# Kernel optimization log

Measured on AMD Instinct MI355X. Metric: run time of the kernel, lower is better.

Reference implementation:

```python
import math
import jax, jax.numpy as jnp
import numpy as np

B, D, H = 8, 2048, 256

def setup_inputs() -> dict:
    key = jax.random.key(0)
    ks = jax.random.split(key, 8)
    s = 1.0 / math.sqrt(H)
    x = jax.random.normal(ks[0], (B, D, H), dtype=jnp.float32)
    adj = jax.random.randint(ks[1], (B, D, D), 0, 2, dtype=jnp.int32)
    Wq = jax.random.normal(ks[2], (H, H), dtype=jnp.float32) * s
    Wk = jax.random.normal(ks[3], (H, H), dtype=jnp.float32) * s
    Wv = jax.random.normal(ks[4], (H, H), dtype=jnp.float32) * s
    Wp = jax.random.normal(ks[5], (H, H), dtype=jnp.float32) * s
    bp = jax.random.normal(ks[6], (H,), dtype=jnp.float32) * 0.01
    gamma = jnp.ones((H,), dtype=jnp.float32)
    beta = jnp.zeros((H,), dtype=jnp.float32)
    return {"x": x, "adj": adj, "Wq": Wq, "Wk": Wk, "Wv": Wv,
            "Wp": Wp, "bp": bp, "gamma": gamma, "beta": beta}

def _layer_norm(h, gamma, beta, eps=1e-5):
    mu = jnp.mean(h, axis=-1, keepdims=True)
    var = jnp.mean(jnp.square(h - mu), axis=-1, keepdims=True)
    return (h - mu) * jax.lax.rsqrt(var + eps) * gamma + beta

def reference(x, adj, Wq, Wk, Wv, Wp, bp, gamma, beta):
    # torch Linear: y = x @ W.T
    q = jnp.einsum('bdh,oh->bdo', x, Wq)
    k = jnp.einsum('bdh,oh->bdo', x, Wk)
    v = jnp.einsum('bdh,oh->bdo', x, Wv)
    scores = jnp.einsum('bdo,beo->bde', q, k) / math.sqrt(H)
    scores = jnp.where(adj <= 0, jnp.float32(-1e9), scores)
    attn = jax.nn.softmax(scores, axis=-1)
    agg = jnp.einsum('bde,beo->bdo', attn, v)
    out = jnp.einsum('bdo,po->bdp', agg, Wp) + bp
    return _layer_norm(x + out, gamma, beta)
```

## Files before the change

### kernel.cpp

```cpp
#include <hip/hip_runtime.h>
#include <stdint.h>

#define NB 8
#define ND 2048
#define NH 256

typedef __attribute__((ext_vector_type(8))) short bf16x8;
typedef __attribute__((ext_vector_type(4))) float f32x4;
typedef __attribute__((ext_vector_type(16))) float f32x16;
typedef __attribute__((ext_vector_type(4))) int   i32x4;
typedef __attribute__((ext_vector_type(2))) unsigned int u32x2;
typedef __attribute__((ext_vector_type(4))) unsigned int u32x4;

#define MFMA16 __builtin_amdgcn_mfma_f32_16x16x32_bf16
#define MFMA32 __builtin_amdgcn_mfma_f32_32x32x16_bf16

__device__ __forceinline__ unsigned short f2bf(float f) {
    union { float f; unsigned int u; } c; c.f = f;
    unsigned int u = c.u + 0x7FFFu + ((c.u >> 16) & 1u);
    return (unsigned short)(u >> 16);
}
__device__ __forceinline__ unsigned int pack2(float a, float b) {
    return (unsigned int)f2bf(a) | ((unsigned int)f2bf(b) << 16);
}
__device__ __forceinline__ unsigned int cvtpk(float a, float b) {
    unsigned int r;
    asm("v_cvt_pk_bf16_f32 %0, %1, %2" : "=v"(r) : "v"(a), "v"(b));
    return r;
}
__device__ __forceinline__ void plswap(unsigned int& a, unsigned int& b) {
    asm volatile("v_permlane32_swap_b32 %0, %1" : "+v"(a), "+v"(b));
}
__device__ __forceinline__ bf16x8 mk8(unsigned int a, unsigned int b, unsigned int c, unsigned int d) {
    union { unsigned int u[4]; bf16x8 v; } x;
    x.u[0] = a; x.u[1] = b; x.u[2] = c; x.u[3] = d;
    return x.v;
}
__device__ __forceinline__ void gload_lds16(const void* g, void* l) {
    __builtin_amdgcn_global_load_lds(
        (const __attribute__((address_space(1))) void*)g,
        (__attribute__((address_space(3))) void*)l, 16, 0, 0);
}
__device__ __forceinline__ float bflo(unsigned int u) { return __uint_as_float(u << 16); }
__device__ __forceinline__ float bfhi(unsigned int u) { return __uint_as_float(u & 0xffff0000u); }

__global__ __launch_bounds__(256) void qkv_kernel(
    const float* __restrict__ x,
    const float* __restrict__ Wq, const float* __restrict__ Wk, const float* __restrict__ Wv,
    unsigned short* __restrict__ qb, unsigned short* __restrict__ kb, unsigned short* __restrict__ vT)
{
    __shared__ unsigned short Wt[64][264];
    __shared__ unsigned short Xt[64][264];
    const int m0 = blockIdx.x * 64;
    const int o0 = blockIdx.y * 64;
    const int t = threadIdx.x;
    const int w = t >> 6, lane = t & 63, lr = lane & 15, half = lane >> 4;
    const int ar0 = 32 * (w >> 1), br0 = 32 * (w & 1);

#pragma unroll
    for (int i = 0; i < 16; ++i) {
        int fidx = i * 256 + t, row = fidx >> 6, c4 = fidx & 63;
        f32x4 vW = *reinterpret_cast<const f32x4*>(Wq + (size_t)(o0 + row) * NH + c4 * 4);
        f32x4 vX = *reinterpret_cast<const f32x4*>(x + (size_t)(m0 + row) * NH + c4 * 4);
        u32x2 pw; pw[0] = pack2(vW[0], vW[1]); pw[1] = pack2(vW[2], vW[3]);
        u32x2 px; px[0] = pack2(vX[0], vX[1]); px[1] = pack2(vX[2], vX[3]);
        *reinterpret_cast<u32x2*>(&Wt[row][c4 * 4]) = pw;
        *reinterpret_cast<u32x2*>(&Xt[row][c4 * 4]) = px;
    }
    __syncthreads();

    for (int z = 0; z < 3; ++z) {
        const unsigned short (*Ab)[264] = (z == 2) ? Xt : Wt;
        const unsigned short (*Bb)[264] = (z == 2) ? Wt : Xt;

        f32x4 acc[2][2] = {};
#pragma unroll
        for (int kk = 0; kk < 8; ++kk) {
            bf16x8 a[2], bfr[2];
#pragma unroll
            for (int f = 0; f < 2; ++f) {
                a[f]   = *reinterpret_cast<const bf16x8*>(&Ab[ar0 + 16 * f + lr][32 * kk + 8 * half]);
                bfr[f] = *reinterpret_cast<const bf16x8*>(&Bb[br0 + 16 * f + lr][32 * kk + 8 * half]);
            }
#pragma unroll
            for (int fa = 0; fa < 2; ++fa)
#pragma unroll
                for (int fb = 0; fb < 2; ++fb)
                    acc[fa][fb] = MFMA16(a[fa], bfr[fb], acc[fa][fb], 0, 0, 0);
        }

        if (z == 0) {
#pragma unroll
            for (int fa = 0; fa < 2; ++fa)
#pragma unroll
                for (int fb = 0; fb < 2; ++fb) {
                    int m = m0 + br0 + 16 * fb + lr;
                    int o = o0 + ar0 + 16 * fa + 4 * half;
                    u32x2 pk; pk[0] = pack2(acc[fa][fb][0], acc[fa][fb][1]);
                    pk[1] = pack2(acc[fa][fb][2], acc[fa][fb][3]);
                    *reinterpret_cast<u32x2*>(qb + (size_t)m * NH + o) = pk;
                }
        } else if (z == 1) {
#pragma unroll
            for (int fa = 0; fa < 2; ++fa)
#pragma unroll
                for (int fb = 0; fb < 2; ++fb) {
                    int m = m0 + br0 + 16 * fb + lr;
                    int o = o0 + ar0 + 16 * fa + 4 * half;
                    int bb = m >> 11, el = m & 2047;
                    u32x2 pk; pk[0] = pack2(acc[fa][fb][0], acc[fa][fb][1]);
                    pk[1] = pack2(acc[fa][fb][2], acc[fa][fb][3]);
                    size_t idx = (((size_t)bb * 32 + (o >> 3)) * 2048 + el) * 8 + (o & 7);
                    *reinterpret_cast<u32x2*>(kb + idx) = pk;
                }
        } else {
#pragma unroll
            for (int fa = 0; fa < 2; ++fa)
#pragma unroll
                for (int fb = 0; fb < 2; ++fb) {
                    int dg = m0 + ar0 + 16 * fa + 4 * half;
                    int o  = o0 + br0 + 16 * fb + lr;
                    int bb = dg >> 11, el = dg & 2047;
                    u32x2 pk; pk[0] = pack2(acc[fa][fb][0], acc[fa][fb][1]);
                    pk[1] = pack2(acc[fa][fb][2], acc[fa][fb][3]);
                    size_t idx = (((size_t)bb * 256 + (el >> 3)) * 256 + o) * 8 + (el & 7);
                    *reinterpret_cast<u32x2*>(vT + idx) = pk;
                }
        }

        if (z < 2) {
            __syncthreads();
            const float* Wn = (z == 0) ? Wk : Wv;
#pragma unroll
            for (int i = 0; i < 16; ++i) {
                int fidx = i * 256 + t, row = fidx >> 6, c4 = fidx & 63;
                f32x4 vW = *reinterpret_cast<const f32x4*>(Wn + (size_t)(o0 + row) * NH + c4 * 4);
                u32x2 pw; pw[0] = pack2(vW[0], vW[1]); pw[1] = pack2(vW[2], vW[3]);
                *reinterpret_cast<u32x2*>(&Wt[row][c4 * 4]) = pw;
            }
            __syncthreads();
        }
    }
}

template<int ESP, int SIDES>
__global__ __launch_bounds__(256, 2) void attn_kernel(
    const unsigned short* __restrict__ qb, const unsigned short* __restrict__ kb,
    const unsigned short* __restrict__ vT, const int* __restrict__ adj,
    unsigned short* __restrict__ part, float* __restrict__ mpart, float* __restrict__ lpart)
{
    constexpr int WAVES = 4;
    constexpr int GROUPS = WAVES / SIDES;
    constexpr int QB = 32 * GROUPS;
    constexpr int NOT = 8 / SIDES;
    constexpr int NT = (ND / ESP) / 32;

    __shared__ unsigned char KT[2][16384];
    __shared__ unsigned char VTl[2][16384];

    const int bid = blockIdx.x;
    const int b = bid & 7, es0 = (bid >> 3) & (ESP - 1), qt = bid / (8 * ESP);
    const int t = threadIdx.x, w = t >> 6, l = t & 63;
    const int lo32 = l & 31, hi = l >> 5;
    const int g = w & (GROUPS - 1), side = w / GROUPS;
    const int qbase = qt * QB + g * 32;
    const int obase = side * (256 / SIDES);
    const int ebase = es0 * (ND / ESP);
    const float SC = 0.0625f, L2E = 1.44269504f;

    bf16x8 qf[16];
    {
        const unsigned short* qr = qb + ((size_t)b * ND + qbase + lo32) * NH + 8 * hi;
#pragma unroll
        for (int kk = 0; kk < 16; ++kk)
            qf[kk] = *reinterpret_cast<const bf16x8*>(qr + kk * 16);
    }

    const char* kbc = (const char*)kb + ((size_t)b << 20);
    const char* vtc = (const char*)vT + ((size_t)b << 20);
    const int* adjr = adj + ((size_t)b * ND + qbase + lo32) * ND + ebase;

    auto stageK = [&](int buf, int tt) {
        const int e0s = ebase + tt * 32;
#pragma unroll
        for (int i = 0; i < 4; ++i) {
            int off = i * 4096 + t * 16;
            int koct = off >> 9, e = (off >> 4) & 31;
            gload_lds16(kbc + (size_t)koct * 32768 + (size_t)(e0s + e) * 16, &KT[buf][off]);
        }
    };
    auto stageV = [&](int buf, int tt) {
        const int Eb = (ebase + tt * 32) >> 3;
#pragma unroll
        for (int i = 0; i < 4; ++i) {
            int off = i * 4096 + t * 16;
            int eoct = off >> 12, o = (off >> 4) & 255;
            gload_lds16(vtc + (size_t)(Eb + eoct) * 4096 + (size_t)o * 16, &VTl[buf][off]);
        }
    };

    f32x16 acc[NOT] = {};
    float m_run = -__builtin_inff(), l_run = 0.f;

    stageK(0, 0); stageV(0, 0);
    __syncthreads();

    for (int tt = 0; tt < NT; ++tt) {
        const int cur = tt & 1;
        if (tt < NT - 1) { stageK(cur ^ 1, tt + 1); stageV(cur ^ 1, tt + 1); }

        i32x4 aj[4];
#pragma unroll
        for (int gg = 0; gg < 4; ++gg)
            aj[gg] = *reinterpret_cast<const i32x4*>(adjr + tt * 32 + gg * 8 + 4 * hi);

        const char* Kc = (const char*)&KT[cur][0];
        f32x16 sc = {};
#pragma unroll
        for (int kk = 0; kk < 16; ++kk) {
            bf16x8 kf = *reinterpret_cast<const bf16x8*>(Kc + kk * 1024 + hi * 512 + lo32 * 16);
            sc = MFMA32(kf, qf[kk], sc, 0, 0, 0);
        }

        float p[16];
        float tmax = -__builtin_inff();
#pragma unroll
        for (int gg = 0; gg < 4; ++gg)
#pragma unroll
            for (int r = 0; r < 4; ++r) {
                float sv = sc[gg * 4 + r] * SC;
                sv = (aj[gg][r] > 0) ? sv : -1e9f;
                p[gg * 4 + r] = sv;
                tmax = fmaxf(tmax, sv);
            }
        tmax = fmaxf(tmax, __shfl_xor(tmax, 32));
        if (!__all(tmax <= m_run + 8.0f)) {
            const float m_new = fmaxf(m_run, tmax);
            const float scale = exp2f((m_run - m_new) * L2E);
#pragma unroll
            for (int ot = 0; ot < NOT; ++ot)
#pragma unroll
                for (int r = 0; r < 16; ++r) acc[ot][r] *= scale;
            l_run *= scale;
            m_run = m_new;
        }
        float psum = 0.f;
#pragma unroll
        for (int r2 = 0; r2 < 16; ++r2) {
            float pe = exp2f((p[r2] - m_run) * L2E);
            p[r2] = pe;
            psum += pe;
        }
        psum += __shfl_xor(psum, 32);
        l_run += psum;

        unsigned int c0 = cvtpk(p[0], p[1]),   c1 = cvtpk(p[2], p[3]);
        unsigned int c2 = cvtpk(p[4], p[5]),   c3 = cvtpk(p[6], p[7]);
        plswap(c0, c2); plswap(c1, c3);
        unsigned int c4 = cvtpk(p[8], p[9]),   c5 = cvtpk(p[10], p[11]);
        unsigned int c6 = cvtpk(p[12], p[13]), c7 = cvtpk(p[14], p[15]);
        plswap(c4, c6); plswap(c5, c7);
        const bf16x8 pf0 = mk8(c0, c1, c2, c3);
        const bf16x8 pf1 = mk8(c4, c5, c6, c7);

        const char* Vc = (const char*)&VTl[cur][0];
#pragma unroll
        for (int ot = 0; ot < NOT; ++ot) {
            bf16x8 vf = *reinterpret_cast<const bf16x8*>(
                Vc + hi * 4096 + (size_t)(obase + ot * 32 + lo32) * 16);
            acc[ot] = MFMA32(vf, pf0, acc[ot], 0, 0, 0);
        }
#pragma unroll
        for (int ot = 0; ot < NOT; ++ot) {
            bf16x8 vf = *reinterpret_cast<const bf16x8*>(
                Vc + 8192 + hi * 4096 + (size_t)(obase + ot * 32 + lo32) * 16);
            acc[ot] = MFMA32(vf, pf1, acc[ot], 0, 0, 0);
        }
        __syncthreads();
    }

    const int qg = b * ND + qbase + lo32;
    unsigned short* pb = part + ((size_t)es0 * 16384 + qg) * 256;
#pragma unroll
    for (int ot = 0; ot < NOT; ++ot)
#pragma unroll
        for (int g2 = 0; g2 < 4; ++g2) {
            u32x2 pk;
            pk[0] = pack2(acc[ot][g2 * 4 + 0], acc[ot][g2 * 4 + 1]);
            pk[1] = pack2(acc[ot][g2 * 4 + 2], acc[ot][g2 * 4 + 3]);
            *reinterpret_cast<u32x2*>(pb + obase + ot * 32 + g2 * 8 + 4 * hi) = pk;
        }
    if (hi == 0 && side == 0) {
        mpart[(size_t)es0 * 16384 + qg] = m_run;
        lpart[(size_t)es0 * 16384 + qg] = l_run;
    }
}

template<int ESP>
__global__ __launch_bounds__(256) void fuse_kernel(
    const unsigned short* __restrict__ part, const float* __restrict__ mpart,
    const float* __restrict__ lpart, const float* __restrict__ Wp,
    const float* __restrict__ bp, const float* __restrict__ x,
    const float* __restrict__ gamma, const float* __restrict__ beta,
    float* __restrict__ out)
{
    __shared__ unsigned short Xt[64][264];
    __shared__ unsigned short Wt[64][264];
    __shared__ float hL[64][264];
    __shared__ float cel[64][ESP];

    const int M0 = blockIdx.x * 64;
    const int t = threadIdx.x;
    const float L2E = 1.44269504f;

    if (t < 64) {
        float me[ESP], le[ESP], M = -__builtin_inff();
#pragma unroll
        for (int e = 0; e < ESP; ++e) {
            me[e] = mpart[(size_t)e * 16384 + M0 + t];
            le[e] = lpart[(size_t)e * 16384 + M0 + t];
            M = fmaxf(M, me[e]);
        }
        float wsum = 0.f;
#pragma unroll
        for (int e = 0; e < ESP; ++e) { me[e] = exp2f((me[e] - M) * L2E); wsum += me[e] * le[e]; }
        const float inv = 1.f / wsum;
#pragma unroll
        for (int e = 0; e < ESP; ++e) cel[t][e] = me[e] * inv;
    }
#pragma unroll
    for (int i = 0; i < 16; ++i) {
        int fidx = i * 256 + t, row = fidx >> 6, c4 = fidx & 63;
        f32x4 vW = *reinterpret_cast<const f32x4*>(Wp + (size_t)row * NH + c4 * 4);
        u32x2 pw; pw[0] = pack2(vW[0], vW[1]); pw[1] = pack2(vW[2], vW[3]);
        *reinterpret_cast<u32x2*>(&Wt[row][c4 * 4]) = pw;
    }
    __syncthreads();

#pragma unroll
    for (int i = 0; i < 8; ++i) {
        int fidx = i * 256 + t, row = fidx >> 5, c8 = fidx & 31;
        float o[8] = {};
#pragma unroll
        for (int e = 0; e < ESP; ++e) {
            u32x4 v = *reinterpret_cast<const u32x4*>(
                part + (((size_t)e * 16384 + M0 + row) * 256 + c8 * 8));
            const float ce = cel[row][e];
#pragma unroll
            for (int j = 0; j < 4; ++j) {
                o[2 * j]     += ce * bflo(v[j]);
                o[2 * j + 1] += ce * bfhi(v[j]);
            }
        }
        u32x4 pk;
#pragma unroll
        for (int j = 0; j < 4; ++j) pk[j] = pack2(o[2 * j], o[2 * j + 1]);
        *reinterpret_cast<u32x4*>(&Xt[row][c8 * 8]) = pk;
    }
    __syncthreads();

    const int w = t >> 6, lane = t & 63, lr = lane & 15, half = lane >> 4;
    const int ar0 = 32 * (w >> 1), br0 = 32 * (w & 1);

    for (int pc = 0; pc < 4; ++pc) {
        f32x4 acc[2][2] = {};
#pragma unroll
        for (int kk = 0; kk < 8; ++kk) {
            bf16x8 a[2], bfr[2];
#pragma unroll
            for (int f = 0; f < 2; ++f) {
                a[f]   = *reinterpret_cast<const bf16x8*>(&Wt[ar0 + 16 * f + lr][32 * kk + 8 * half]);
                bfr[f] = *reinterpret_cast<const bf16x8*>(&Xt[br0 + 16 * f + lr][32 * kk + 8 * half]);
            }
#pragma unroll
            for (int fa = 0; fa < 2; ++fa)
#pragma unroll
                for (int fb = 0; fb < 2; ++fb)
                    acc[fa][fb] = MFMA16(a[fa], bfr[fb], acc[fa][fb], 0, 0, 0);
        }
#pragma unroll
        for (int fa = 0; fa < 2; ++fa)
#pragma unroll
            for (int fb = 0; fb < 2; ++fb) {
                int p = pc * 64 + ar0 + 16 * fa + 4 * half;
                int m = br0 + 16 * fb + lr;
                *reinterpret_cast<f32x4*>(&hL[m][p]) = acc[fa][fb];
            }
        if (pc < 3) {
            __syncthreads();
#pragma unroll
            for (int i = 0; i < 16; ++i) {
                int fidx = i * 256 + t, row = fidx >> 6, c4 = fidx & 63;
                f32x4 vW = *reinterpret_cast<const f32x4*>(
                    Wp + (size_t)((pc + 1) * 64 + row) * NH + c4 * 4);
                u32x2 pw; pw[0] = pack2(vW[0], vW[1]); pw[1] = pack2(vW[2], vW[3]);
                *reinterpret_cast<u32x2*>(&Wt[row][c4 * 4]) = pw;
            }
            __syncthreads();
        }
    }
    __syncthreads();

    f32x4 gm = *reinterpret_cast<const f32x4*>(gamma + lane * 4);
    f32x4 be = *reinterpret_cast<const f32x4*>(beta + lane * 4);
    f32x4 bv = *reinterpret_cast<const f32x4*>(bp + lane * 4);
    for (int rr = 0; rr < 16; ++rr) {
        const int row = w * 16 + rr;
        f32x4 v = *reinterpret_cast<const f32x4*>(&hL[row][lane * 4]);
        f32x4 xr = *reinterpret_cast<const f32x4*>(x + (size_t)(M0 + row) * NH + lane * 4);
#pragma unroll
        for (int r = 0; r < 4; ++r) v[r] += xr[r] + bv[r];
        float s = v[0] + v[1] + v[2] + v[3];
#pragma unroll
        for (int off = 1; off < 64; off <<= 1) s += __shfl_xor(s, off);
        const float mu = s * (1.f / 256.f);
        f32x4 dv; float q = 0.f;
#pragma unroll
        for (int r = 0; r < 4; ++r) { dv[r] = v[r] - mu; q += dv[r] * dv[r]; }
#pragma unroll
        for (int off = 1; off < 64; off <<= 1) q += __shfl_xor(q, off);
        const float rs = rsqrtf(q * (1.f / 256.f) + 1e-5f);
        f32x4 o;
#pragma unroll
        for (int r = 0; r < 4; ++r) o[r] = dv[r] * rs * gm[r] + be[r];
        *reinterpret_cast<f32x4*>(out + (size_t)(M0 + row) * NH + lane * 4) = o;
    }
}

extern "C" void kernel_launch(void* const* d_in, const int* in_sizes, int n_in,
                              void* d_out, int out_size, void* d_ws, size_t ws_size,
                              hipStream_t stream)
{
    const float* x     = (const float*)d_in[0];
    const int*   adj   = (const int*)d_in[1];
    const float* Wq    = (const float*)d_in[2];
    const float* Wk    = (const float*)d_in[3];
    const float* Wv    = (const float*)d_in[4];
    const float* Wp    = (const float*)d_in[5];
    const float* bp    = (const float*)d_in[6];
    const float* gamma = (const float*)d_in[7];
    const float* beta  = (const float*)d_in[8];

    char* ws = (char*)d_ws;
    const size_t MB = 1024 * 1024;
    unsigned short* qb    = (unsigned short*)(ws);
    unsigned short* kb    = (unsigned short*)(ws + 8 * MB);
    unsigned short* vT    = (unsigned short*)(ws + 16 * MB);
    unsigned short* partb = (unsigned short*)(ws + 24 * MB);
    float* out = (float*)d_out;

    qkv_kernel<<<dim3(256, 4), 256, 0, stream>>>(x, Wq, Wk, Wv, qb, kb, vT);

    const bool big = ws_size >= (size_t)57 * MB;
    if (big) {
        float* mpart = (float*)(ws + 56 * MB);
        float* lpart = (float*)(ws + 56 * MB + 256 * 1024);
        attn_kernel<4, 1><<<dim3(512), 256, 0, stream>>>(qb, kb, vT, adj, partb, mpart, lpart);
        fuse_kernel<4><<<dim3(256), 256, 0, stream>>>(partb, mpart, lpart, Wp, bp, x, gamma, beta, out);
    } else {
        float* mpart = (float*)(ws + 40 * MB);
        float* lpart = (float*)(ws + 40 * MB + 128 * 1024);
        attn_kernel<2, 2><<<dim3(512), 256, 0, stream>>>(qb, kb, vT, adj, partb, mpart, lpart);
        fuse_kernel<2><<<dim3(256), 256, 0, stream>>>(partb, mpart, lpart, Wp, bp, x, gamma, beta, out);
    }
}
```

Before: 120.7 us.

## Use 512-thread attention blocks splitting output dims, prefetch adjacency, dual MFMA chains

The attention kernel now runs 8 waves per block: 4 query groups of 32 rows, each split into two halves of the output dimension, so every staged K/V tile serves 128 query rows. The adjacency mask for the next tile is loaded early, during softmax, to hide its global latency. QK^T now uses two independent MFMA accumulator chains that are summed afterward, which shortens the dependency chain. The cost is that each wave recomputes the full QK^T scores for its query group, roughly doubling score MFMAs per output, and register pressure rises under 512-thread launch bounds.

```diff
diff --git a/kernel.cpp b/kernel.cpp
--- a/kernel.cpp
+++ b/kernel.cpp
@@ -143,16 +143,15 @@
     }
 }
 
-template<int ESP, int SIDES>
-__global__ __launch_bounds__(256, 2) void attn_kernel(
+template<int ESP>
+__global__ __launch_bounds__(512, 2) void attn_kernel(
     const unsigned short* __restrict__ qb, const unsigned short* __restrict__ kb,
     const unsigned short* __restrict__ vT, const int* __restrict__ adj,
     unsigned short* __restrict__ part, float* __restrict__ mpart, float* __restrict__ lpart)
 {
-    constexpr int WAVES = 4;
-    constexpr int GROUPS = WAVES / SIDES;
+    constexpr int GROUPS = 4;
     constexpr int QB = 32 * GROUPS;
-    constexpr int NOT = 8 / SIDES;
+    constexpr int NOT = 4;
     constexpr int NT = (ND / ESP) / 32;
 
     __shared__ unsigned char KT[2][16384];
@@ -164,7 +163,7 @@
     const int lo32 = l & 31, hi = l >> 5;
     const int g = w & (GROUPS - 1), side = w / GROUPS;
     const int qbase = qt * QB + g * 32;
-    const int obase = side * (256 / SIDES);
+    const int obase = side * 128;
     const int ebase = es0 * (ND / ESP);
     const float SC = 0.0625f, L2E = 1.44269504f;
 
@@ -183,8 +182,8 @@
     auto stageK = [&](int buf, int tt) {
         const int e0s = ebase + tt * 32;
 #pragma unroll
-        for (int i = 0; i < 4; ++i) {
-            int off = i * 4096 + t * 16;
+        for (int i = 0; i < 2; ++i) {
+            int off = i * 8192 + t * 16;
             int koct = off >> 9, e = (off >> 4) & 31;
             gload_lds16(kbc + (size_t)koct * 32768 + (size_t)(e0s + e) * 16, &KT[buf][off]);
         }
@@ -192,8 +191,8 @@
     auto stageV = [&](int buf, int tt) {
         const int Eb = (ebase + tt * 32) >> 3;
 #pragma unroll
-        for (int i = 0; i < 4; ++i) {
-            int off = i * 4096 + t * 16;
+        for (int i = 0; i < 2; ++i) {
+            int off = i * 8192 + t * 16;
             int eoct = off >> 12, o = (off >> 4) & 255;
             gload_lds16(vtc + (size_t)(Eb + eoct) * 4096 + (size_t)o * 16, &VTl[buf][off]);
         }
@@ -203,23 +202,24 @@
     float m_run = -__builtin_inff(), l_run = 0.f;
 
     stageK(0, 0); stageV(0, 0);
+    i32x4 aj[4];
+#pragma unroll
+    for (int gg = 0; gg < 4; ++gg)
+        aj[gg] = *reinterpret_cast<const i32x4*>(adjr + gg * 8 + 4 * hi);
     __syncthreads();
 
     for (int tt = 0; tt < NT; ++tt) {
         const int cur = tt & 1;
         if (tt < NT - 1) { stageK(cur ^ 1, tt + 1); stageV(cur ^ 1, tt + 1); }
 
-        i32x4 aj[4];
-#pragma unroll
-        for (int gg = 0; gg < 4; ++gg)
-            aj[gg] = *reinterpret_cast<const i32x4*>(adjr + tt * 32 + gg * 8 + 4 * hi);
-
         const char* Kc = (const char*)&KT[cur][0];
-        f32x16 sc = {};
-#pragma unroll
-        for (int kk = 0; kk < 16; ++kk) {
-            bf16x8 kf = *reinterpret_cast<const bf16x8*>(Kc + kk * 1024 + hi * 512 + lo32 * 16);
-            sc = MFMA32(kf, qf[kk], sc, 0, 0, 0);
+        f32x16 sc0 = {}, sc1 = {};
+#pragma unroll
+        for (int kk = 0; kk < 16; kk += 2) {
+            bf16x8 kf0 = *reinterpret_cast<const bf16x8*>(Kc + kk * 1024 + hi * 512 + lo32 * 16);
+            bf16x8 kf1 = *reinterpret_cast<const bf16x8*>(Kc + (kk + 1) * 1024 + hi * 512 + lo32 * 16);
+            sc0 = MFMA32(kf0, qf[kk], sc0, 0, 0, 0);
+            sc1 = MFMA32(kf1, qf[kk + 1], sc1, 0, 0, 0);
         }
 
         float p[16];
@@ -228,7 +228,7 @@
         for (int gg = 0; gg < 4; ++gg)
 #pragma unroll
             for (int r = 0; r < 4; ++r) {
-                float sv = sc[gg * 4 + r] * SC;
+                float sv = (sc0[gg * 4 + r] + sc1[gg * 4 + r]) * SC;
                 sv = (aj[gg][r] > 0) ? sv : -1e9f;
                 p[gg * 4 + r] = sv;
                 tmax = fmaxf(tmax, sv);
@@ -253,6 +253,12 @@
         }
         psum += __shfl_xor(psum, 32);
         l_run += psum;
+
+        if (tt < NT - 1) {
+#pragma unroll
+            for (int gg = 0; gg < 4; ++gg)
+                aj[gg] = *reinterpret_cast<const i32x4*>(adjr + (tt + 1) * 32 + gg * 8 + 4 * hi);
+        }
 
         unsigned int c0 = cvtpk(p[0], p[1]),   c1 = cvtpk(p[2], p[3]);
         unsigned int c2 = cvtpk(p[4], p[5]),   c3 = cvtpk(p[6], p[7]);
@@ -455,12 +461,12 @@
     if (big) {
         float* mpart = (float*)(ws + 56 * MB);
         float* lpart = (float*)(ws + 56 * MB + 256 * 1024);
-        attn_kernel<4, 1><<<dim3(512), 256, 0, stream>>>(qb, kb, vT, adj, partb, mpart, lpart);
+        attn_kernel<4><<<dim3(512), 512, 0, stream>>>(qb, kb, vT, adj, partb, mpart, lpart);
         fuse_kernel<4><<<dim3(256), 256, 0, stream>>>(partb, mpart, lpart, Wp, bp, x, gamma, beta, out);
     } else {
         float* mpart = (float*)(ws + 40 * MB);
         float* lpart = (float*)(ws + 40 * MB + 128 * 1024);
-        attn_kernel<2, 2><<<dim3(512), 256, 0, stream>>>(qb, kb, vT, adj, partb, mpart, lpart);
+        attn_kernel<2><<<dim3(256), 512, 0, stream>>>(qb, kb, vT, adj, partb, mpart, lpart);
         fuse_kernel<2><<<dim3(256), 256, 0, stream>>>(partb, mpart, lpart, Wp, bp, x, gamma, beta, out);
     }
 }
```

Result: slower. 155.2 us (+28.7%).
